# Kernel optimization log

Measured on AMD Instinct MI355X. Metric: run time of the kernel, lower is better.

Reference implementation:

```python
import jax, jax.numpy as jnp
import numpy as np

B, N_DET, N_T, NY, NX = 4, 128, 2048, 256, 256


def setup_inputs() -> dict:
    key = jax.random.key(0)
    k1, k2, k3 = jax.random.split(key, 3)
    sino = jax.random.normal(k1, (B, 1, N_DET, N_T), dtype=jnp.float32)
    # LUT channel 0: floor temporal index (stored as float, cast to int in forward)
    k_floor = jax.random.randint(k2, (NY, NX, N_DET), 0, N_T).astype(jnp.float32)
    # LUT channel 1: linear interpolation weight alpha in [0,1)
    alpha = jax.random.uniform(k3, (NY, NX, N_DET), dtype=jnp.float32)
    lut = jnp.stack([k_floor, alpha], axis=-1)  # [NY, NX, N_DET, 2]
    return {"sino": sino, "lut": lut}


def reference(sino, lut):
    # sino: [B, 1, n_det, n_t]; lut: [ny, nx, n_det, 2]
    b, c, n_det, n_t = sino.shape
    k_floor = lut[..., 0].astype(jnp.int32)          # [ny, nx, n_det]
    alpha = lut[..., 1]                               # [ny, nx, n_det]
    valid = (k_floor >= 0) & (k_floor < n_t - 1)
    k0 = jnp.clip(k_floor, 0, n_t - 2)
    k1 = k0 + 1
    S = sino[:, 0]                                    # [B, n_det, n_t]
    det = jnp.arange(n_det)                           # broadcasts against [ny,nx,n_det]
    s0 = S[:, det, k0]                                # [B, ny, nx, n_det]
    s1 = S[:, det, k1]                                # [B, ny, nx, n_det]
    sk = (1.0 - alpha) * s0 + alpha * s1
    sk = jnp.where(valid, sk, jnp.zeros_like(sk))
    # Hann apodization window over detectors
    apod = (0.5 - 0.5 * jnp.cos(2.0 * jnp.pi * jnp.arange(n_det, dtype=jnp.float32)
                                / max(n_det - 1, 1))).astype(sino.dtype)
    out = jnp.einsum('bijd,d->bij', sk, apod)
    norm = jnp.maximum(apod.sum(), 1e-06)
    out = out / norm
    return out[:, None]                               # [B, 1, ny, nx]
```

## Files before the change

### kernel.cpp

```cpp
#include <hip/hip_runtime.h>
#include <hip/hip_fp16.h>


#define NB      4
#define NDET    128
#define NT      2048
#define NPIX    65536
#define DBLOCK  8
#define DPH     2
#define NPHASE  4
#define PTILE   1024
#define THREADS 512
#define PXPT    (PTILE / THREADS)

__global__ __launch_bounds__(256)
void cvt_kernel(const float* __restrict__ sino, uint2* __restrict__ ws16) {
    const int id = blockIdx.x * 256 + threadIdx.x;
    float v0 = sino[id];
    float v1 = sino[id + NDET * NT];
    float v2 = sino[id + 2 * NDET * NT];
    float v3 = sino[id + 3 * NDET * NT];
    __half2 h01 = __floats2half2_rn(v0, v1);
    __half2 h23 = __floats2half2_rn(v2, v3);
    uint2 u;
    u.x = *(const unsigned*)&h01;
    u.y = *(const unsigned*)&h23;
    ws16[id] = u;
}

__global__ __launch_bounds__(THREADS, 4)
void bp_kernel(const uint2* __restrict__ ws16,
               const float* __restrict__ lut,
               float* __restrict__ out) {
    __shared__ uint2 lds2[DPH * NT];

    const int tid   = threadIdx.x;
    const int octet = blockIdx.x & 15;
    const int tile  = blockIdx.x >> 4;
    const int d0    = octet * DBLOCK;
    const int px0   = tile * PTILE;

    float apod[DBLOCK];
#pragma unroll
    for (int j = 0; j < DBLOCK; ++j) {
        float x = (float)(d0 + j) * (6.28318530717958647692f / 127.0f);
        apod[j] = 0.5f - 0.5f * __cosf(x);
    }

    float4 L[PXPT][NPHASE];
#pragma unroll
    for (int i = 0; i < PXPT; ++i) {
        const float4* lp = (const float4*)
            (lut + ((size_t)(px0 + tid + i * THREADS) * NDET + d0) * 2);
#pragma unroll
        for (int q = 0; q < NPHASE; ++q) L[i][q] = lp[q];
    }

    float acc[PXPT][NB];
#pragma unroll
    for (int i = 0; i < PXPT; ++i)
#pragma unroll
        for (int b = 0; b < NB; ++b) acc[i][b] = 0.0f;

    for (int ph = 0; ph < NPHASE; ++ph) {
        const int dg0 = d0 + ph * DPH;
        if (ph) __syncthreads();

        {
            const uint4* src = (const uint4*)(ws16 + (size_t)dg0 * NT);
            uint4* dst = (uint4*)lds2;
            for (int f = tid; f < DPH * NT / 2; f += THREADS)
                dst[f] = src[f];
        }
        __syncthreads();

#pragma unroll
        for (int i = 0; i < PXPT; ++i) {
            float4 Lq = L[i][ph];
#pragma unroll
            for (int h = 0; h < 2; ++h) {
                float kf = h ? Lq.z : Lq.x;
                float af = h ? Lq.w : Lq.y;
                int k = (int)kf;
                bool valid = (unsigned)k < (unsigned)(NT - 1);
                float w  = valid ? apod[ph * DPH + h] : 0.0f;
                int  k0  = valid ? k : 0;
                uint2 e0 = lds2[h * NT + k0];
                uint2 e1 = lds2[h * NT + k0 + 1];
                __half2 a01 = *(__half2*)&e0.x, a23 = *(__half2*)&e0.y;
                __half2 b01 = *(__half2*)&e1.x, b23 = *(__half2*)&e1.y;
                __half2 a2  = __float2half2_rn(af);
                __half2 s01 = __hfma2(a2, __hsub2(b01, a01), a01);
                __half2 s23 = __hfma2(a2, __hsub2(b23, a23), a23);
                float2 f01 = __half22float2(s01);
                float2 f23 = __half22float2(s23);
                acc[i][0] = fmaf(w, f01.x, acc[i][0]);
                acc[i][1] = fmaf(w, f01.y, acc[i][1]);
                acc[i][2] = fmaf(w, f23.x, acc[i][2]);
                acc[i][3] = fmaf(w, f23.y, acc[i][3]);
            }
        }
    }

    const float inv_norm = 1.0f / 63.5f;
#pragma unroll
    for (int i = 0; i < PXPT; ++i) {
        const int px = px0 + tid + i * THREADS;
#pragma unroll
        for (int b = 0; b < NB; ++b) {
            atomicAdd(&out[(size_t)b * NPIX + px], acc[i][b] * inv_norm);
        }
    }
}

__global__ __launch_bounds__(THREADS, 4)
void bp_fallback(const float* __restrict__ sino,
                 const float* __restrict__ lut,
                 float* __restrict__ out) {
    __shared__ __half2 lds[4][NT];
    const int tid   = threadIdx.x;
    const int octet = blockIdx.x & 15;
    const int tile  = blockIdx.x >> 4;
    const int d0    = octet * DBLOCK;
    const int px0   = tile * PTILE;
    float apod[DBLOCK];
#pragma unroll
    for (int j = 0; j < DBLOCK; ++j) {
        float x = (float)(d0 + j) * (6.28318530717958647692f / 127.0f);
        apod[j] = 0.5f - 0.5f * __cosf(x);
    }
    float4 L[PXPT][4];
#pragma unroll
    for (int i = 0; i < PXPT; ++i) {
        const float4* lp = (const float4*)
            (lut + ((size_t)(px0 + tid + i * THREADS) * NDET + d0) * 2);
#pragma unroll
        for (int q = 0; q < 4; ++q) L[i][q] = lp[q];
    }
    float acc[PXPT][NB];
#pragma unroll
    for (int i = 0; i < PXPT; ++i)
#pragma unroll
        for (int b = 0; b < NB; ++b) acc[i][b] = 0.0f;
    const float4* s4 = (const float4*)sino;
    for (int ph = 0; ph < 4; ++ph) {
        const int b0  = (ph >> 1) * 2;
        const int dh  = ph & 1;
        const int dg0 = d0 + dh * 4;
        if (ph) __syncthreads();
        for (int f = tid; f < 4 * (NT / 4); f += THREADS) {
            int dl = f >> 9;
            int t4 = f & 511;
            size_t row = ((size_t)b0 * NDET + dg0 + dl) * (NT / 4) + t4;
            float4 ve = s4[row];
            float4 vo = s4[row + (size_t)NDET * (NT / 4)];
            __half2* dstp = &lds[dl][t4 * 4];
            dstp[0] = __floats2half2_rn(ve.x, vo.x);
            dstp[1] = __floats2half2_rn(ve.y, vo.y);
            dstp[2] = __floats2half2_rn(ve.z, vo.z);
            dstp[3] = __floats2half2_rn(ve.w, vo.w);
        }
        __syncthreads();
#pragma unroll
        for (int i = 0; i < PXPT; ++i) {
#pragma unroll
            for (int q2 = 0; q2 < 2; ++q2) {
                float4 Lq = L[i][dh * 2 + q2];
#pragma unroll
                for (int h = 0; h < 2; ++h) {
                    float kf = h ? Lq.z : Lq.x;
                    float af = h ? Lq.w : Lq.y;
                    int   dl = q2 * 2 + h;
                    int k = (int)kf;
                    bool valid = (unsigned)k < (unsigned)(NT - 1);
                    float w  = valid ? apod[dh * 4 + dl] : 0.0f;
                    int  k0  = valid ? k : 0;
                    __half2 s0v = lds[dl][k0];
                    __half2 s1v = lds[dl][k0 + 1];
                    __half2 a2  = __float2half2_rn(af);
                    __half2 sk  = __hfma2(a2, __hsub2(s1v, s0v), s0v);
                    float2  fv  = __half22float2(sk);
                    acc[i][b0 + 0] = fmaf(w, fv.x, acc[i][b0 + 0]);
                    acc[i][b0 + 1] = fmaf(w, fv.y, acc[i][b0 + 1]);
                }
            }
        }
    }
    const float inv_norm = 1.0f / 63.5f;
#pragma unroll
    for (int i = 0; i < PXPT; ++i) {
        const int px = px0 + tid + i * THREADS;
#pragma unroll
        for (int b = 0; b < NB; ++b)
            atomicAdd(&out[(size_t)b * NPIX + px], acc[i][b] * inv_norm);
    }
}

extern "C" void kernel_launch(void* const* d_in, const int* in_sizes, int n_in,
                              void* d_out, int out_size, void* d_ws, size_t ws_size,
                              hipStream_t stream) {
    const float* sino = (const float*)d_in[0];
    const float* lut  = (const float*)d_in[1];
    float* out = (float*)d_out;

    (void)hipMemsetAsync(d_out, 0, (size_t)out_size * sizeof(float), stream);

    const size_t ws_needed = (size_t)NDET * NT * sizeof(uint2);
    if (ws_size >= ws_needed) {
        uint2* ws16 = (uint2*)d_ws;
        cvt_kernel<<<dim3(NDET * NT / 256), dim3(256), 0, stream>>>(sino, ws16);
        bp_kernel<<<dim3(1024), dim3(THREADS), 0, stream>>>(ws16, lut, out);
    } else {
        bp_fallback<<<dim3(1024), dim3(THREADS), 0, stream>>>(sino, lut, out);
    }
}
```

Before: 124.3 us.

## Use larger pixel tiles and 4-detector LDS phases with deferred LUT loads

The backprojection block grows to 1024 threads covering 2048 pixels. Each phase now stages 4 detector rows of the packed fp16 sinogram into LDS (64KB), so there are 2 phases per block instead of 4 and fewer barriers. The LUT entries for the second phase are loaded after the first LDS fill, which defers their latency and lowers live registers early in the kernel. In exchange, per-block LDS use and block size grow, which can reduce occupancy. The launch bound of (1024, 4) may also force register limits or spills.

```diff
diff --git a/kernel.cpp b/kernel.cpp
--- a/kernel.cpp
+++ b/kernel.cpp
@@ -7,10 +7,9 @@
 #define NT      2048
 #define NPIX    65536
 #define DBLOCK  8
-#define DPH     2
-#define NPHASE  4
-#define PTILE   1024
-#define THREADS 512
+#define DQ      4
+#define PTILE   2048
+#define THREADS 1024
 #define PXPT    (PTILE / THREADS)
 
 __global__ __launch_bounds__(256)
@@ -32,7 +31,7 @@
 void bp_kernel(const uint2* __restrict__ ws16,
                const float* __restrict__ lut,
                float* __restrict__ out) {
-    __shared__ uint2 lds2[DPH * NT];
+    __shared__ uint2 lds2[DQ * NT];
 
     const int tid   = threadIdx.x;
     const int octet = blockIdx.x & 15;
@@ -47,60 +46,85 @@
         apod[j] = 0.5f - 0.5f * __cosf(x);
     }
 
-    float4 L[PXPT][NPHASE];
+    float acc[PXPT][NB];
+#pragma unroll
+    for (int i = 0; i < PXPT; ++i)
+#pragma unroll
+        for (int b = 0; b < NB; ++b) acc[i][b] = 0.0f;
+
+    const float4* lp[PXPT];
+#pragma unroll
+    for (int i = 0; i < PXPT; ++i)
+        lp[i] = (const float4*)
+            (lut + ((size_t)(px0 + tid + i * THREADS) * NDET + d0) * 2);
+
+    float4 Lcur[PXPT][2];
 #pragma unroll
     for (int i = 0; i < PXPT; ++i) {
-        const float4* lp = (const float4*)
-            (lut + ((size_t)(px0 + tid + i * THREADS) * NDET + d0) * 2);
-#pragma unroll
-        for (int q = 0; q < NPHASE; ++q) L[i][q] = lp[q];
-    }
-
-    float acc[PXPT][NB];
-#pragma unroll
-    for (int i = 0; i < PXPT; ++i)
-#pragma unroll
-        for (int b = 0; b < NB; ++b) acc[i][b] = 0.0f;
-
-    for (int ph = 0; ph < NPHASE; ++ph) {
-        const int dg0 = d0 + ph * DPH;
-        if (ph) __syncthreads();
-
-        {
-            const uint4* src = (const uint4*)(ws16 + (size_t)dg0 * NT);
-            uint4* dst = (uint4*)lds2;
-            for (int f = tid; f < DPH * NT / 2; f += THREADS)
-                dst[f] = src[f];
-        }
-        __syncthreads();
-
+        Lcur[i][0] = lp[i][0];
+        Lcur[i][1] = lp[i][1];
+    }
+
+    {
+        const uint4* src = (const uint4*)(ws16 + (size_t)d0 * NT);
+        uint4* dst = (uint4*)lds2;
+#pragma unroll
+        for (int r = 0; r < 4; ++r) dst[tid + r * THREADS] = src[tid + r * THREADS];
+    }
+    __syncthreads();
+
+    float4 Lnext[PXPT][2];
+#pragma unroll
+    for (int i = 0; i < PXPT; ++i) {
+        Lnext[i][0] = lp[i][2];
+        Lnext[i][1] = lp[i][3];
+    }
+
+    auto gather = [&](const float4 (*Lq)[2], int jbase) {
 #pragma unroll
         for (int i = 0; i < PXPT; ++i) {
-            float4 Lq = L[i][ph];
-#pragma unroll
-            for (int h = 0; h < 2; ++h) {
-                float kf = h ? Lq.z : Lq.x;
-                float af = h ? Lq.w : Lq.y;
-                int k = (int)kf;
-                bool valid = (unsigned)k < (unsigned)(NT - 1);
-                float w  = valid ? apod[ph * DPH + h] : 0.0f;
-                int  k0  = valid ? k : 0;
-                uint2 e0 = lds2[h * NT + k0];
-                uint2 e1 = lds2[h * NT + k0 + 1];
-                __half2 a01 = *(__half2*)&e0.x, a23 = *(__half2*)&e0.y;
-                __half2 b01 = *(__half2*)&e1.x, b23 = *(__half2*)&e1.y;
-                __half2 a2  = __float2half2_rn(af);
-                __half2 s01 = __hfma2(a2, __hsub2(b01, a01), a01);
-                __half2 s23 = __hfma2(a2, __hsub2(b23, a23), a23);
-                float2 f01 = __half22float2(s01);
-                float2 f23 = __half22float2(s23);
-                acc[i][0] = fmaf(w, f01.x, acc[i][0]);
-                acc[i][1] = fmaf(w, f01.y, acc[i][1]);
-                acc[i][2] = fmaf(w, f23.x, acc[i][2]);
-                acc[i][3] = fmaf(w, f23.y, acc[i][3]);
+#pragma unroll
+            for (int q = 0; q < 2; ++q) {
+                float4 Le = Lq[i][q];
+#pragma unroll
+                for (int h = 0; h < 2; ++h) {
+                    float kf = h ? Le.z : Le.x;
+                    float af = h ? Le.w : Le.y;
+                    int   dl = q * 2 + h;
+                    int k = (int)kf;
+                    bool valid = (unsigned)k < (unsigned)(NT - 1);
+                    float w  = valid ? apod[jbase + dl] : 0.0f;
+                    int  k0  = valid ? k : 0;
+                    uint2 e0 = lds2[dl * NT + k0];
+                    uint2 e1 = lds2[dl * NT + k0 + 1];
+                    __half2 a01 = *(__half2*)&e0.x, a23 = *(__half2*)&e0.y;
+                    __half2 b01 = *(__half2*)&e1.x, b23 = *(__half2*)&e1.y;
+                    __half2 a2  = __float2half2_rn(af);
+                    __half2 s01 = __hfma2(a2, __hsub2(b01, a01), a01);
+                    __half2 s23 = __hfma2(a2, __hsub2(b23, a23), a23);
+                    float2 f01 = __half22float2(s01);
+                    float2 f23 = __half22float2(s23);
+                    acc[i][0] = fmaf(w, f01.x, acc[i][0]);
+                    acc[i][1] = fmaf(w, f01.y, acc[i][1]);
+                    acc[i][2] = fmaf(w, f23.x, acc[i][2]);
+                    acc[i][3] = fmaf(w, f23.y, acc[i][3]);
+                }
             }
         }
-    }
+    };
+
+    gather(Lcur, 0);
+    __syncthreads();
+
+    {
+        const uint4* src = (const uint4*)(ws16 + (size_t)(d0 + DQ) * NT);
+        uint4* dst = (uint4*)lds2;
+#pragma unroll
+        for (int r = 0; r < 4; ++r) dst[tid + r * THREADS] = src[tid + r * THREADS];
+    }
+    __syncthreads();
+
+    gather(Lnext, DQ);
 
     const float inv_norm = 1.0f / 63.5f;
 #pragma unroll
@@ -113,7 +137,7 @@
     }
 }
 
-__global__ __launch_bounds__(THREADS, 4)
+__global__ __launch_bounds__(512, 4)
 void bp_fallback(const float* __restrict__ sino,
                  const float* __restrict__ lut,
                  float* __restrict__ out) {
@@ -122,24 +146,24 @@
     const int octet = blockIdx.x & 15;
     const int tile  = blockIdx.x >> 4;
     const int d0    = octet * DBLOCK;
-    const int px0   = tile * PTILE;
+    const int px0   = tile * 1024;
     float apod[DBLOCK];
 #pragma unroll
     for (int j = 0; j < DBLOCK; ++j) {
         float x = (float)(d0 + j) * (6.28318530717958647692f / 127.0f);
         apod[j] = 0.5f - 0.5f * __cosf(x);
     }
-    float4 L[PXPT][4];
-#pragma unroll
-    for (int i = 0; i < PXPT; ++i) {
-        const float4* lp = (const float4*)
-            (lut + ((size_t)(px0 + tid + i * THREADS) * NDET + d0) * 2);
-#pragma unroll
-        for (int q = 0; q < 4; ++q) L[i][q] = lp[q];
-    }
-    float acc[PXPT][NB];
-#pragma unroll
-    for (int i = 0; i < PXPT; ++i)
+    float4 L[2][4];
+#pragma unroll
+    for (int i = 0; i < 2; ++i) {
+        const float4* lq = (const float4*)
+            (lut + ((size_t)(px0 + tid + i * 512) * NDET + d0) * 2);
+#pragma unroll
+        for (int q = 0; q < 4; ++q) L[i][q] = lq[q];
+    }
+    float acc[2][NB];
+#pragma unroll
+    for (int i = 0; i < 2; ++i)
 #pragma unroll
         for (int b = 0; b < NB; ++b) acc[i][b] = 0.0f;
     const float4* s4 = (const float4*)sino;
@@ -148,7 +172,7 @@
         const int dh  = ph & 1;
         const int dg0 = d0 + dh * 4;
         if (ph) __syncthreads();
-        for (int f = tid; f < 4 * (NT / 4); f += THREADS) {
+        for (int f = tid; f < 4 * (NT / 4); f += 512) {
             int dl = f >> 9;
             int t4 = f & 511;
             size_t row = ((size_t)b0 * NDET + dg0 + dl) * (NT / 4) + t4;
@@ -162,7 +186,7 @@
         }
         __syncthreads();
 #pragma unroll
-        for (int i = 0; i < PXPT; ++i) {
+        for (int i = 0; i < 2; ++i) {
 #pragma unroll
             for (int q2 = 0; q2 < 2; ++q2) {
                 float4 Lq = L[i][dh * 2 + q2];
@@ -188,8 +212,8 @@
     }
     const float inv_norm = 1.0f / 63.5f;
 #pragma unroll
-    for (int i = 0; i < PXPT; ++i) {
-        const int px = px0 + tid + i * THREADS;
+    for (int i = 0; i < 2; ++i) {
+        const int px = px0 + tid + i * 512;
 #pragma unroll
         for (int b = 0; b < NB; ++b)
             atomicAdd(&out[(size_t)b * NPIX + px], acc[i][b] * inv_norm);
@@ -209,8 +233,8 @@
     if (ws_size >= ws_needed) {
         uint2* ws16 = (uint2*)d_ws;
         cvt_kernel<<<dim3(NDET * NT / 256), dim3(256), 0, stream>>>(sino, ws16);
-        bp_kernel<<<dim3(1024), dim3(THREADS), 0, stream>>>(ws16, lut, out);
+        bp_kernel<<<dim3(512), dim3(THREADS), 0, stream>>>(ws16, lut, out);
     } else {
-        bp_fallback<<<dim3(1024), dim3(THREADS), 0, stream>>>(sino, lut, out);
-    }
-}
+        bp_fallback<<<dim3(1024), dim3(512), 0, stream>>>(sino, lut, out);
+    }
+}
```

Result: no change. 123.6 us (-0.6%).
